# Kernel optimization log

Measured on AMD Instinct MI355X. Metric: run time of the kernel, lower is better.

The kernel has to match this reference:

```python
import jax, jax.numpy as jnp
import numpy as np

TEX_H = 256
TEX_W = 256
F_CH = 16
D_FACTOR = 0.5
DECAY = float(np.sqrt(2.0 * D_FACTOR * D_FACTOR))           # sqrt(d^2 + d^2)
AF = int(-np.log(0.1) * DECAY + 0.5)                        # active_field = 2
K = 2 * AF                                                  # 4x4 splat window


def setup_inputs() -> dict:
    key = jax.random.key(0)
    k1, k2, k3 = jax.random.split(key, 3)
    B, H, W = 8, 256, 256
    f_map = jax.random.normal(k1, (B, H, W, F_CH), dtype=jnp.float32)
    uv_map = jax.random.uniform(k2, (B, H, W, 2), dtype=jnp.float32)   # uv in [0,1)
    mask = (jax.random.uniform(k3, (B, H, W, 1)) < 0.5).astype(jnp.float32)
    return {"f_map": f_map, "uv_map": uv_map, "mask": mask}


def reference(f_map, uv_map, mask):
    B, H, W, C = f_map.shape
    N = B * H * W
    # uv_map[..., ::-1] * [tex_h, tex_w]: v comes from channel 1, u from channel 0
    v = (uv_map[..., 1] * TEX_H).reshape(N)
    u = (uv_map[..., 0] * TEX_W).reshape(N)
    pix = f_map.reshape(N, C)
    m = mask.reshape(N)  # 1 = masked pixel contributes (TF gathers where mask==1)

    v_shift = jnp.maximum(v - AF, 0.0)
    u_shift = jnp.maximum(u - AF, 0.0)
    offs = jnp.arange(K, dtype=jnp.float32)
    v_grid = v_shift[:, None, None] + offs[None, :, None]   # [N,K,K]
    u_grid = u_shift[:, None, None] + offs[None, None, :]   # [N,K,K]

    du = jnp.abs(u_grid - u[:, None, None])
    du = jnp.minimum(du, jnp.abs(du - TEX_W))               # wrap-around distance
    dv = jnp.abs(v_grid - v[:, None, None])
    dv = jnp.minimum(dv, jnp.abs(dv - TEX_H))
    wmap = jnp.exp(-jnp.sqrt(du * du + dv * dv) / DECAY)
    wmap = wmap * (wmap > 0.1) * m[:, None, None]           # threshold + mask gating

    vi = v_grid.astype(jnp.int32)
    ui = u_grid.astype(jnp.int32)
    valid = (vi < TEX_H) & (ui < TEX_W)                     # drop out-of-range splats
    wmap = wmap * valid
    idx = (jnp.clip(vi, 0, TEX_H - 1) * TEX_W + jnp.clip(ui, 0, TEX_W - 1)).reshape(-1)

    w_flat = wmap.reshape(-1)                               # [N*K*K]
    vals = (wmap.reshape(N, K * K)[..., None] * pix[:, None, :]).reshape(-1, C)

    wsum = jnp.zeros((TEX_H * TEX_W,), jnp.float32).at[idx].add(w_flat)
    csum = jnp.zeros((TEX_H * TEX_W, C), jnp.float32).at[idx].add(vals)
    wsum = wsum.reshape(TEX_H, TEX_W, 1)
    csum = csum.reshape(TEX_H, TEX_W, C)

    tex = (csum * (wsum > 0.01)) / (wsum + 0.001)           # weighted average
    return jnp.broadcast_to(tex[None], (B, TEX_H, TEX_W, C))
```

## Files before the change

kernel.cpp:

```cpp
#include <hip/hip_runtime.h>
#include <hip/hip_fp16.h>

#define TEX_H 256
#define TEX_W 256
#define FCH 16
#define NPIX (8 * 256 * 256)
#define NCELL (256 * 256)

#define SQRT2_F 1.41421356237f
#define W_EDGE   0.24311673443f
#define W_DIAG   0.13533528324f

typedef float vf4 __attribute__((ext_vector_type(4)));

#define HALO_OFF   0
#define DIR_C_OFF  (NCELL * 64)
#define DIR_W_OFF  (DIR_C_OFF + 2048 * 16 * 4)
#define ZERO_BYTES (DIR_W_OFF + 2048 * 4)

__global__ __launch_bounds__(256) void splat_kernel(
    const float*  __restrict__ f_map,
    const float2* __restrict__ uv_map,
    const float*  __restrict__ mask,
    char* __restrict__ wsb)
{
    __half2* halo = (__half2*)(wsb + HALO_OFF);
    float*   dirc = (float*)  (wsb + DIR_C_OFF);
    float*   dirw = (float*)  (wsb + DIR_W_OFF);

    int tid = blockIdx.x * 256 + threadIdx.x;
    int pix = tid >> 3;
    int l   = tid & 7;

    if (mask[pix] == 0.0f) return;

    float2 uv = uv_map[pix];
    float u = uv.x * 256.0f;
    float v = uv.y * 256.0f;

    if (u >= 2.0f && v >= 2.0f) {
        int cell = ((int)v) * 256 + (int)u;
        float2 fp = ((const float2*)f_map)[(size_t)pix * 8 + l];
        __half2 h = __floats2half2_rn(fp.x, fp.y);
        __half2* hp = halo + (size_t)cell * 16;
        unsafeAtomicAdd(&hp[l], h);
        if (l == 0) unsafeAtomicAdd(&hp[8], __floats2half2_rn(1.0f, 0.0f));
    } else {
        float fa = f_map[(size_t)pix * FCH + l];
        float fb = f_map[(size_t)pix * FCH + l + 8];
        float us = fmaxf(u - 2.0f, 0.0f);
        float vs = fmaxf(v - 2.0f, 0.0f);
        #pragma unroll
        for (int kv = 0; kv < 4; ++kv) {
            float vg = vs + (float)kv;
            int vi = (int)vg;
            float dvf = fabsf(vg - v);
            #pragma unroll
            for (int ku = 0; ku < 4; ++ku) {
                float ug = us + (float)ku;
                int ui = (int)ug;
                float duf = fabsf(ug - u);
                float w = expf(-sqrtf(duf * duf + dvf * dvf) * SQRT2_F);
                if (w > 0.1f && vi < TEX_H && ui < TEX_W) {
                    int cell = (ui < 4) ? (ui * 256 + vi)
                                        : ((4 + vi) * 256 + ui);
                    unsafeAtomicAdd(&dirc[(size_t)cell * FCH + l],     w * fa);
                    unsafeAtomicAdd(&dirc[(size_t)cell * FCH + l + 8], w * fb);
                    if (l == 0) unsafeAtomicAdd(&dirw[cell], w);
                }
            }
        }
    }
}

__global__ __launch_bounds__(256) void finalize_kernel(
    const char* __restrict__ wsb,
    float* __restrict__ out)
{
    const __half2* halo = (const __half2*)(wsb + HALO_OFF);
    const float*   dirc = (const float*)  (wsb + DIR_C_OFF);
    const float*   dirw = (const float*)  (wsb + DIR_W_OFF);

    __shared__ __half2 s_h[100][8];
    __shared__ float   s_n[100];

    int tile = blockIdx.x;
    int r0 = (tile >> 5) << 3;
    int c0 = (tile & 31) << 3;

    int i = threadIdx.x;
    if (i < 200) {
        int cellIdx = i >> 1, part = i & 1;
        int hr = cellIdx / 10, hc = cellIdx - hr * 10;
        int gr = r0 + hr - 1, gc = c0 + hc - 1;
        uint4 val = make_uint4(0, 0, 0, 0);
        bool inb = (gr >= 0) & (gr < 256) & (gc >= 0) & (gc < 256);
        size_t gcell = inb ? ((size_t)gr * 256 + gc) : 0;
        if (inb)
            val = *(const uint4*)(halo + gcell * 16 + part * 4);
        *(uint4*)&s_h[cellIdx][part * 4] = val;
        if (part == 0)
            s_n[cellIdx] = inb ? __low2float(halo[gcell * 16 + 8]) : 0.0f;
    }
    __syncthreads();

    int tx = threadIdx.x >> 2;
    int c4 = threadIdx.x & 3;
    int lr = tx >> 3, lc = tx & 7;
    int gr = r0 + lr, gc = c0 + lc;

    vf4 cs = {0.f, 0.f, 0.f, 0.f};
    float wsm = 0.0f;

    #pragma unroll
    for (int a = 0; a < 3; ++a) {
        #pragma unroll
        for (int b = 0; b < 3; ++b) {
            float w = (a == 1 && b == 1) ? 1.0f
                    : ((a == 1 || b == 1) ? W_EDGE : W_DIAG);
            int idx = (lr + a) * 10 + (lc + b);
            float2 f0 = __half22float2(s_h[idx][c4 * 2 + 0]);
            float2 f1 = __half22float2(s_h[idx][c4 * 2 + 1]);
            cs.x += w * f0.x; cs.y += w * f0.y;
            cs.z += w * f1.x; cs.w += w * f1.y;
            wsm  += w * s_n[idx];
        }
    }

    if (gc < 4) {
        int cell = gc * 256 + gr;
        cs += *(const vf4*)&dirc[(size_t)cell * FCH + c4 * 4];
        wsm += dirw[cell];
    } else if (gr < 4) {
        int cell = (4 + gr) * 256 + gc;
        cs += *(const vf4*)&dirc[(size_t)cell * FCH + c4 * 4];
        wsm += dirw[cell];
    }

    float s = (wsm > 0.01f) ? (1.0f / (wsm + 0.001f)) : 0.0f;
    cs *= s;

    size_t base = ((size_t)gr * 256 + gc) * FCH + c4 * 4;
    #pragma unroll
    for (int b = 0; b < 8; ++b) {
        __builtin_nontemporal_store(cs, (vf4*)&out[(size_t)b * (256 * 256 * FCH) + base]);
    }
}

extern "C" void kernel_launch(void* const* d_in, const int* in_sizes, int n_in,
                              void* d_out, int out_size, void* d_ws, size_t ws_size,
                              hipStream_t stream) {
    const float*  f_map  = (const float*)d_in[0];
    const float2* uv_map = (const float2*)d_in[1];
    const float*  mask   = (const float*)d_in[2];
    float* out = (float*)d_out;
    char*  wsb = (char*)d_ws;

    (void)hipMemsetAsync(wsb, 0, (size_t)ZERO_BYTES, stream);

    splat_kernel<<<(NPIX * 8) / 256, 256, 0, stream>>>(f_map, uv_map, mask, wsb);
    finalize_kernel<<<1024, 256, 0, stream>>>(wsb, out);
}
```

Baseline: 62.05 us.

## Bin splats by row slab then accumulate per-slab in shared memory

Replaces the direct global half2 atomic splat with a two-pass scheme. A binning kernel writes packed pixel entries into fixed-capacity per-block slab buckets and spills overflow to global atomics. An accumulation kernel then gathers the features for each half-slab into shared memory with LDS atomics and flushes them once to global. This targets the heavy contention and traffic of global atomics, at the cost of an extra launch, an entry buffer, and scattered f_map gathers. The count now lives in a separate float array instead of the half2 slot.

Result: slower. 105.2 us (+69.5%).

```diff
diff --git a/kernel.cpp b/kernel.cpp
--- a/kernel.cpp
+++ b/kernel.cpp
@@ -6,6 +6,12 @@
 #define FCH 16
 #define NPIX (8 * 256 * 256)
 #define NCELL (256 * 256)
+#define NBLKA 1024
+#define NSLAB 64
+#define SLABCELLS 1024
+#define HALFCELLS 512
+#define BCAP 20
+#define BSTRIDE 24
 
 #define SQRT2_F 1.41421356237f
 #define W_EDGE   0.24311673443f
@@ -13,63 +19,164 @@
 
 typedef float vf4 __attribute__((ext_vector_type(4)));
 
-#define HALO_OFF   0
-#define DIR_C_OFF  (NCELL * 64)
-#define DIR_W_OFF  (DIR_C_OFF + 2048 * 16 * 4)
-#define ZERO_BYTES (DIR_W_OFF + 2048 * 4)
-
-__global__ __launch_bounds__(256) void splat_kernel(
+#define ENT_OFF_B  0
+#define HALO_OFF_B (NBLKA * NSLAB * BSTRIDE * 4)
+#define HCNT_OFF_B (HALO_OFF_B + NCELL * 32)
+#define DIRC_OFF_B (HCNT_OFF_B + NCELL * 4)
+#define DIRW_OFF_B (DIRC_OFF_B + 2048 * 64)
+#define WS_END_B   (DIRW_OFF_B + 2048 * 4)
+
+__device__ __forceinline__ void boundary_splat16(float u, float v, int pix,
+                                                 const float* __restrict__ f_map,
+                                                 float* __restrict__ dirc,
+                                                 float* __restrict__ dirw) {
+    float fv[16];
+    #pragma unroll
+    for (int i = 0; i < 4; ++i) {
+        vf4 x = *(const vf4*)(f_map + (size_t)pix * FCH + i * 4);
+        fv[i*4+0]=x.x; fv[i*4+1]=x.y; fv[i*4+2]=x.z; fv[i*4+3]=x.w;
+    }
+    float us = fmaxf(u - 2.0f, 0.0f);
+    float vs = fmaxf(v - 2.0f, 0.0f);
+    for (int kv = 0; kv < 4; ++kv) {
+        float vg = vs + (float)kv;
+        int vi = (int)vg;
+        float dvf = fabsf(vg - v);
+        for (int ku = 0; ku < 4; ++ku) {
+            float ug = us + (float)ku;
+            int ui = (int)ug;
+            float duf = fabsf(ug - u);
+            float w = expf(-sqrtf(duf * duf + dvf * dvf) * SQRT2_F);
+            if (w > 0.1f && vi < TEX_H && ui < TEX_W) {
+                int cell = (ui < 4) ? (ui * 256 + vi)
+                                    : ((4 + vi) * 256 + ui);
+                float* p = dirc + (size_t)cell * FCH;
+                #pragma unroll
+                for (int i = 0; i < 16; ++i) unsafeAtomicAdd(p + i, w * fv[i]);
+                unsafeAtomicAdd(dirw + cell, w);
+            }
+        }
+    }
+}
+
+__device__ __forceinline__ void overflow_splat(int pix, int cell,
+                                               const float* __restrict__ f_map,
+                                               __half2* __restrict__ halo,
+                                               float* __restrict__ hcnt) {
+    #pragma unroll
+    for (int j = 0; j < 8; ++j) {
+        float2 fp = ((const float2*)f_map)[(size_t)pix * 8 + j];
+        unsafeAtomicAdd(&halo[(size_t)cell * 8 + j], __floats2half2_rn(fp.x, fp.y));
+    }
+    unsafeAtomicAdd(&hcnt[cell], 1.0f);
+}
+
+__global__ __launch_bounds__(256) void bin2_kernel(
     const float*  __restrict__ f_map,
     const float2* __restrict__ uv_map,
     const float*  __restrict__ mask,
     char* __restrict__ wsb)
 {
-    __half2* halo = (__half2*)(wsb + HALO_OFF);
-    float*   dirc = (float*)  (wsb + DIR_C_OFF);
-    float*   dirw = (float*)  (wsb + DIR_W_OFF);
-
-    int tid = blockIdx.x * 256 + threadIdx.x;
-    int pix = tid >> 3;
-    int l   = tid & 7;
-
-    if (mask[pix] == 0.0f) return;
-
-    float2 uv = uv_map[pix];
-    float u = uv.x * 256.0f;
-    float v = uv.y * 256.0f;
-
-    if (u >= 2.0f && v >= 2.0f) {
-        int cell = ((int)v) * 256 + (int)u;
-        float2 fp = ((const float2*)f_map)[(size_t)pix * 8 + l];
-        __half2 h = __floats2half2_rn(fp.x, fp.y);
-        __half2* hp = halo + (size_t)cell * 16;
-        unsafeAtomicAdd(&hp[l], h);
-        if (l == 0) unsafeAtomicAdd(&hp[8], __floats2half2_rn(1.0f, 0.0f));
-    } else {
-        float fa = f_map[(size_t)pix * FCH + l];
-        float fb = f_map[(size_t)pix * FCH + l + 8];
-        float us = fmaxf(u - 2.0f, 0.0f);
-        float vs = fmaxf(v - 2.0f, 0.0f);
-        #pragma unroll
-        for (int kv = 0; kv < 4; ++kv) {
-            float vg = vs + (float)kv;
-            int vi = (int)vg;
-            float dvf = fabsf(vg - v);
-            #pragma unroll
-            for (int ku = 0; ku < 4; ++ku) {
-                float ug = us + (float)ku;
-                int ui = (int)ug;
-                float duf = fabsf(ug - u);
-                float w = expf(-sqrtf(duf * duf + dvf * dvf) * SQRT2_F);
-                if (w > 0.1f && vi < TEX_H && ui < TEX_W) {
-                    int cell = (ui < 4) ? (ui * 256 + vi)
-                                        : ((4 + vi) * 256 + ui);
-                    unsafeAtomicAdd(&dirc[(size_t)cell * FCH + l],     w * fa);
-                    unsafeAtomicAdd(&dirc[(size_t)cell * FCH + l + 8], w * fb);
-                    if (l == 0) unsafeAtomicAdd(&dirw[cell], w);
-                }
+    __shared__ int s_hist[NSLAB];
+    int t = threadIdx.x;
+    if (t < NSLAB) s_hist[t] = 0;
+    __syncthreads();
+
+    unsigned* ent = (unsigned*)(wsb + ENT_OFF_B) + (size_t)blockIdx.x * NSLAB * BSTRIDE;
+    __half2*  halo = (__half2*)(wsb + HALO_OFF_B);
+    float*    hcnt = (float*)  (wsb + HCNT_OFF_B);
+    float*    dirc = (float*)  (wsb + DIRC_OFF_B);
+    float*    dirw = (float*)  (wsb + DIRW_OFF_B);
+
+    #pragma unroll
+    for (int k = 0; k < 2; ++k) {
+        int pix = blockIdx.x * 512 + k * 256 + t;
+        if (mask[pix] != 0.0f) {
+            float2 uv = uv_map[pix];
+            float u = uv.x * 256.0f;
+            float v = uv.y * 256.0f;
+            if (u >= 2.0f && v >= 2.0f) {
+                int iu = (int)u, iv = (int)v;
+                int slab = iv >> 2;
+                int cl   = ((iv & 3) << 8) | iu;
+                int slot = atomicAdd(&s_hist[slab], 1);
+                if (slot < BCAP)
+                    ent[slab * BSTRIDE + 1 + slot] = ((unsigned)cl << 19) | (unsigned)pix;
+                else
+                    overflow_splat(pix, iv * 256 + iu, f_map, halo, hcnt);
+            } else {
+                boundary_splat16(u, v, pix, f_map, dirc, dirw);
             }
         }
+    }
+    __syncthreads();
+    if (t < NSLAB) ent[t * BSTRIDE] = (unsigned)min(s_hist[t], BCAP);
+}
+
+__global__ __launch_bounds__(512) void accum_kernel(
+    const float* __restrict__ f_map,
+    char* __restrict__ wsb)
+{
+    __shared__ float s_halo[HALFCELLS][FCH];
+    __shared__ float s_cnt[HALFCELLS];
+
+    for (int i = threadIdx.x; i < HALFCELLS * FCH; i += 512) ((float*)s_halo)[i] = 0.0f;
+    for (int i = threadIdx.x; i < HALFCELLS;       i += 512) s_cnt[i] = 0.0f;
+    __syncthreads();
+
+    int slab = blockIdx.x >> 2;
+    int h    = (blockIdx.x >> 1) & 1;
+    int q    = blockIdx.x & 1;
+    int g = threadIdx.x >> 4;
+    int c = threadIdx.x & 15;
+
+    const unsigned* entbase = (const unsigned*)(wsb + ENT_OFF_B);
+
+    for (int b = q * 512 + g; b < (q + 1) * 512; b += 32) {
+        const unsigned* buck = entbase + ((size_t)b * NSLAB + slab) * BSTRIDE;
+        unsigned wA = buck[c];
+        unsigned wB = (c < 8) ? buck[16 + c] : 0u;
+        int count = (int)__shfl(wA, 0, 16);
+
+        for (int e = 1; e <= count; e += 4) {
+            int e1 = min(e + 1, count), e2 = min(e + 2, count), e3 = min(e + 3, count);
+            unsigned x0 = (e  < 16) ? __shfl(wA, e,  16) : __shfl(wB, e  - 16, 16);
+            unsigned x1 = (e1 < 16) ? __shfl(wA, e1, 16) : __shfl(wB, e1 - 16, 16);
+            unsigned x2 = (e2 < 16) ? __shfl(wA, e2, 16) : __shfl(wB, e2 - 16, 16);
+            unsigned x3 = (e3 < 16) ? __shfl(wA, e3, 16) : __shfl(wB, e3 - 16, 16);
+            bool v0 = ((x0 >> 28) & 1) == (unsigned)h;
+            bool v1 = (e + 1 <= count) && (((x1 >> 28) & 1) == (unsigned)h);
+            bool v2 = (e + 2 <= count) && (((x2 >> 28) & 1) == (unsigned)h);
+            bool v3 = (e + 3 <= count) && (((x3 >> 28) & 1) == (unsigned)h);
+            float f0 = v0 ? f_map[(size_t)(x0 & 0x7FFFFu) * FCH + c] : 0.0f;
+            float f1 = v1 ? f_map[(size_t)(x1 & 0x7FFFFu) * FCH + c] : 0.0f;
+            float f2 = v2 ? f_map[(size_t)(x2 & 0x7FFFFu) * FCH + c] : 0.0f;
+            float f3 = v3 ? f_map[(size_t)(x3 & 0x7FFFFu) * FCH + c] : 0.0f;
+            if (v0) atomicAdd(&s_halo[(x0 >> 19) & 511][c], f0);
+            if (v1) atomicAdd(&s_halo[(x1 >> 19) & 511][c], f1);
+            if (v2) atomicAdd(&s_halo[(x2 >> 19) & 511][c], f2);
+            if (v3) atomicAdd(&s_halo[(x3 >> 19) & 511][c], f3);
+            if (c == 0) {
+                if (v0) atomicAdd(&s_cnt[(x0 >> 19) & 511], 1.0f);
+                if (v1) atomicAdd(&s_cnt[(x1 >> 19) & 511], 1.0f);
+                if (v2) atomicAdd(&s_cnt[(x2 >> 19) & 511], 1.0f);
+                if (v3) atomicAdd(&s_cnt[(x3 >> 19) & 511], 1.0f);
+            }
+        }
+    }
+    __syncthreads();
+
+    __half2* halo = (__half2*)(wsb + HALO_OFF_B);
+    float*   hcnt = (float*)  (wsb + HCNT_OFF_B);
+    size_t cbase = (size_t)slab * SLABCELLS + (size_t)h * HALFCELLS;
+    for (int i = threadIdx.x; i < HALFCELLS * 8; i += 512) {
+        int cell = i >> 3, wp = i & 7;
+        float a = s_halo[cell][wp * 2], bb = s_halo[cell][wp * 2 + 1];
+        unsafeAtomicAdd(&halo[(cbase + cell) * 8 + wp], __floats2half2_rn(a, bb));
+    }
+    for (int i = threadIdx.x; i < HALFCELLS; i += 512) {
+        float n = s_cnt[i];
+        if (n != 0.0f) unsafeAtomicAdd(&hcnt[cbase + i], n);
     }
 }
 
@@ -77,9 +184,10 @@
     const char* __restrict__ wsb,
     float* __restrict__ out)
 {
-    const __half2* halo = (const __half2*)(wsb + HALO_OFF);
-    const float*   dirc = (const float*)  (wsb + DIR_C_OFF);
-    const float*   dirw = (const float*)  (wsb + DIR_W_OFF);
+    const __half2* halo = (const __half2*)(wsb + HALO_OFF_B);
+    const float*   hcnt = (const float*)  (wsb + HCNT_OFF_B);
+    const float*   dirc = (const float*)  (wsb + DIRC_OFF_B);
+    const float*   dirw = (const float*)  (wsb + DIRW_OFF_B);
 
     __shared__ __half2 s_h[100][8];
     __shared__ float   s_n[100];
@@ -97,10 +205,9 @@
         bool inb = (gr >= 0) & (gr < 256) & (gc >= 0) & (gc < 256);
         size_t gcell = inb ? ((size_t)gr * 256 + gc) : 0;
         if (inb)
-            val = *(const uint4*)(halo + gcell * 16 + part * 4);
+            val = *(const uint4*)(halo + gcell * 8 + part * 4);
         *(uint4*)&s_h[cellIdx][part * 4] = val;
-        if (part == 0)
-            s_n[cellIdx] = inb ? __low2float(halo[gcell * 16 + 8]) : 0.0f;
+        if (part == 0) s_n[cellIdx] = inb ? hcnt[gcell] : 0.0f;
     }
     __syncthreads();
 
@@ -156,8 +263,9 @@
     float* out = (float*)d_out;
     char*  wsb = (char*)d_ws;
 
-    (void)hipMemsetAsync(wsb, 0, (size_t)ZERO_BYTES, stream);
-
-    splat_kernel<<<(NPIX * 8) / 256, 256, 0, stream>>>(f_map, uv_map, mask, wsb);
+    (void)hipMemsetAsync(wsb + HALO_OFF_B, 0, (size_t)(WS_END_B - HALO_OFF_B), stream);
+
+    bin2_kernel<<<NBLKA, 256, 0, stream>>>(f_map, uv_map, mask, wsb);
+    accum_kernel<<<NSLAB * 2 * 2, 512, 0, stream>>>(f_map, wsb);
     finalize_kernel<<<1024, 256, 0, stream>>>(wsb, out);
 }
```
